# Kernel tuning notes

Measured on AMD Instinct MI355X. Metric: run time of the kernel, lower is better.

The kernel has to match this reference:

```python
import jax, jax.numpy as jnp
import numpy as np

B, S, H, NH, L, INTER, WIN = 2, 2048, 512, 8, 4, 2048, 64
HD = H // NH
W1 = WIN // 2          # one-sided window
WB = 2 * W1 + 1        # band width per query
EPS = 1e-12


def layer_norm(x, g, b):
    m = jnp.mean(x, axis=-1, keepdims=True)
    v = jnp.var(x, axis=-1, keepdims=True)
    return (x - m) / jnp.sqrt(v + EPS) * g + b


def setup_inputs() -> dict:
    key = jax.random.key(0)
    ks = jax.random.split(key, 12)
    std = 0.02
    n = lambda k, sh: jax.random.normal(k, sh, jnp.float32) * std
    return {
        "input_embs": jax.random.normal(ks[0], (B, S, H), jnp.float32),
        "attention_mask": jnp.ones((B, S), jnp.float32),
        "pos_emb": n(ks[1], (S, H)),
        "ln_emb_g": jnp.ones((H,), jnp.float32),
        "ln_emb_b": jnp.zeros((H,), jnp.float32),
        "Wq": n(ks[2], (L, H, H)), "bq": jnp.zeros((L, H), jnp.float32),
        "Wk": n(ks[3], (L, H, H)), "bk": jnp.zeros((L, H), jnp.float32),
        "Wv": n(ks[4], (L, H, H)), "bv": jnp.zeros((L, H), jnp.float32),
        "Wo": n(ks[5], (L, H, H)), "bo": jnp.zeros((L, H), jnp.float32),
        "ln1_g": jnp.ones((L, H), jnp.float32), "ln1_b": jnp.zeros((L, H), jnp.float32),
        "Wi": n(ks[6], (L, H, INTER)), "bi": jnp.zeros((L, INTER), jnp.float32),
        "Wo2": n(ks[7], (L, INTER, H)), "bo2": jnp.zeros((L, H), jnp.float32),
        "ln2_g": jnp.ones((L, H), jnp.float32), "ln2_b": jnp.zeros((L, H), jnp.float32),
        "pool_W1": n(ks[8], (H, H)), "pool_b1": jnp.zeros((H,), jnp.float32),
        "pool_W2": n(ks[9], (H, 1)), "pool_b2": jnp.zeros((1,), jnp.float32),
    }


def reference(input_embs, attention_mask, pos_emb, ln_emb_g, ln_emb_b,
              Wq, bq, Wk, bk, Wv, bv, Wo, bo, ln1_g, ln1_b,
              Wi, bi, Wo2, bo2, ln2_g, ln2_b,
              pool_W1, pool_b1, pool_W2, pool_b2):
    # extended additive mask: 0 for attend, -10000 for pad (no global tokens)
    ext = (1.0 - attention_mask) * -10000.0          # [B,S]
    is_masked = ext < 0                              # masked query positions

    # embeddings: input + position, LayerNorm (dropout is identity in eval)
    x = layer_norm(input_embs + pos_emb[None], ln_emb_g, ln_emb_b)

    # sliding-window band indices
    offs = jnp.arange(-W1, W1 + 1)
    idx = jnp.arange(S)[:, None] + offs[None, :]     # [S,WB]
    valid = (idx >= 0) & (idx < S)
    idxc = jnp.clip(idx, 0, S - 1)
    key_bias = ext[:, idxc]                          # [B,S,WB] additive key mask
    scale = 1.0 / jnp.sqrt(jnp.float32(HD))

    def layer(h, p):
        (wq, bq_, wk, bk_, wv, bv_, wo, bo_, g1, b1,
         wi, bi_, wo2, bo2_, g2, b2) = p
        q = (h @ wq + bq_).reshape(B, S, NH, HD) * scale
        k = (h @ wk + bk_).reshape(B, S, NH, HD)
        v = (h @ wv + bv_).reshape(B, S, NH, HD)
        kb = k[:, idxc]                              # [B,S,WB,NH,HD]
        vb = v[:, idxc]
        sc = jnp.einsum('bshd,bswhd->bhsw', q, kb) + key_bias[:, None]
        sc = jnp.where(valid[None, None], sc, -jnp.inf)
        pr = jax.nn.softmax(sc, axis=-1)
        pr = jnp.where(is_masked[:, None, :, None], 0.0, pr)
        ctx = jnp.einsum('bhsw,bswhd->bshd', pr, vb).reshape(B, S, H)
        attn = layer_norm(ctx @ wo + bo_ + h, g1, b1)          # BertSelfOutput
        inter = jax.nn.gelu(attn @ wi + bi_, approximate=False)  # BertIntermediate
        out = layer_norm(inter @ wo2 + bo2_ + attn, g2, b2)      # BertOutput
        return out, None

    params = (Wq, bq, Wk, bk, Wv, bv, Wo, bo, ln1_g, ln1_b,
              Wi, bi, Wo2, bo2, ln2_g, ln2_b)
    x, _ = jax.lax.scan(jax.checkpoint(layer), x, params)

    # AttentionPooling
    e = jnp.tanh(x @ pool_W1 + pool_b1)
    alpha = jnp.exp(e @ pool_W2 + pool_b2) * attention_mask[..., None]  # [B,S,1]
    alpha = alpha / (jnp.sum(alpha, axis=1, keepdims=True) + 1e-8)
    return jnp.einsum('bsh,bs->bh', x, alpha[..., 0])  # [B,H]
```

## Files before the change

kernel.cpp:

```cpp
#include <hip/hip_runtime.h>
#include <hip/hip_bf16.h>
#include <math.h>

#define B_ 2
#define S_ 2048
#define H_ 512
#define NH_ 8
#define HD_ 64
#define L_ 4
#define INTER_ 2048
#define W1_ 32
#define WB_ 65
#define M_ (B_*S_)

typedef __attribute__((ext_vector_type(8))) short short8v;
typedef __attribute__((ext_vector_type(4))) float f32x4;

__device__ __forceinline__ float b2f(ushort u){ return __uint_as_float(((unsigned)u)<<16); }
__device__ __forceinline__ ushort f2b(float f){
  unsigned u = __float_as_uint(f);
  unsigned r = (u + 0x7fffu + ((u>>16)&1u)) >> 16;
  return (ushort)r;
}

__device__ __forceinline__ void async16(const ushort* g, ushort* l){
  __builtin_amdgcn_global_load_lds(
      (const __attribute__((address_space(1))) unsigned int*)g,
      (__attribute__((address_space(3))) unsigned int*)l, 16, 0, 0);
}

__device__ __forceinline__ void tr_tile(const float* __restrict__ src,
    ushort* __restrict__ dst, int R, int C, int r0, int c0)
{
  __shared__ ushort tile[32][33];
  int tx = threadIdx.x & 31, ty = threadIdx.x >> 5;
  #pragma unroll
  for (int i = 0; i < 4; ++i){
    int r = r0 + ty + i*8;
    tile[ty + i*8][tx] = f2b(src[(size_t)r * C + c0 + tx]);
  }
  __syncthreads();
  #pragma unroll
  for (int i = 0; i < 4; ++i){
    int c = c0 + ty + i*8;
    dst[(size_t)c * R + r0 + tx] = tile[tx][ty + i*8];
  }
}

struct TPack {
  const float* wq; const float* wk; const float* wv;
  const float* wo; const float* pw1;
  ushort* wqkvT; ushort* woT; ushort* pw1T;
};

__global__ __launch_bounds__(256) void transpose512_all(TPack p)
{
  int z = blockIdx.z;
  const float* src; ushort* dst;
  if (z < 12){
    int kind = z >> 2, l = z & 3;
    const float* s3[3] = {p.wq, p.wk, p.wv};
    src = s3[kind] + (size_t)l*512*512;
    dst = p.wqkvT + (size_t)l*1536*512 + (size_t)kind*512*512;
  } else if (z < 16){
    int l = z - 12;
    src = p.wo + (size_t)l*512*512;
    dst = p.woT + (size_t)l*512*512;
  } else {
    src = p.pw1; dst = p.pw1T;
  }
  tr_tile(src, dst, 512, 512, blockIdx.y*32, blockIdx.x*32);
}

__global__ __launch_bounds__(256) void transpose_k(const float* __restrict__ src,
    ushort* __restrict__ dst, int R, int C, size_t sBatch, size_t dBatch)
{
  src += (size_t)blockIdx.z * sBatch;
  dst += (size_t)blockIdx.z * dBatch;
  tr_tile(src, dst, R, C, blockIdx.y*32, blockIdx.x*32);
}

__global__ __launch_bounds__(256) void pack_bqkv(const float* __restrict__ bq,
    const float* __restrict__ bk, const float* __restrict__ bv, float* __restrict__ dst)
{
  int i = blockIdx.x * 256 + threadIdx.x;
  int l = i / 1536, n = i % 1536;
  float v = (n < 512) ? bq[l*512 + n] : (n < 1024 ? bk[l*512 + n - 512] : bv[l*512 + n - 1024]);
  dst[i] = v;
}

template<int EPI, int BM>
__global__ __launch_bounds__(256, (BM == 64) ? 4 : 3) void gemm_bt(
    const ushort* __restrict__ A, const ushort* __restrict__ Bt,
    const float* __restrict__ bias, ushort* __restrict__ o16,
    float* __restrict__ o32, int M, int N, int K, int Klen)
{
  constexpr int ABUF = BM * 32;
  constexpr int BUFE = ABUF + 4096;
  constexpr int MI = BM / 32;
  constexpr int AL = BM / 64;
  __shared__ ushort lds[3 * BUFE];
  const int tid = threadIdx.x;
  const int bm = blockIdx.y * BM, bn = blockIdx.x * 128;
  const int kbeg = blockIdx.z * Klen;
  const int wave = tid >> 6, lane = tid & 63;
  const int wr = (wave >> 1) * (BM / 2), wc = (wave & 1) * 64;
  const int lr = lane & 15, lg = lane >> 4;
  const int lkS = (lg ^ ((lr >> 1) & 3)) * 8;
  f32x4 acc[MI][4] = {};

  const int srow = tid >> 2;
  const int schk = (((tid & 3) ^ ((tid >> 3) & 3))) * 8;
  const ushort* Ag  = A  + (size_t)(bm + srow) * K + kbeg + schk;
  const ushort* Bg0 = Bt + (size_t)(bn + srow) * K + kbeg + schk;
  const ushort* Bg1 = Bt + (size_t)(bn + 64 + srow) * K + kbeg + schk;

  const int nIter = Klen >> 5;
  auto issueTile = [&](int t, int buf){
    int k0 = t << 5;
    ushort* d = &lds[0] + buf*BUFE + tid*8;
    #pragma unroll
    for (int r = 0; r < AL; ++r)
      async16(Ag + (size_t)r*64*K + k0, d + r*2048);
    async16(Bg0 + k0, d + ABUF);
    async16(Bg1 + k0, d + ABUF + 2048);
  };

  issueTile(0, 0);
  issueTile(1, 1);

  int cb = 0;
  for (int t = 0; t < nIter; ++t){
    int ib = cb + 2; if (ib >= 3) ib -= 3;
    if (t + 2 < nIter) issueTile(t + 2, ib);
    if constexpr (BM == 64){
      if (t + 2 < nIter)      asm volatile("s_waitcnt vmcnt(6)" ::: "memory");
      else if (t + 1 < nIter) asm volatile("s_waitcnt vmcnt(3)" ::: "memory");
      else                    asm volatile("s_waitcnt vmcnt(0)" ::: "memory");
    } else {
      if (t + 2 < nIter)      asm volatile("s_waitcnt vmcnt(8)" ::: "memory");
      else if (t + 1 < nIter) asm volatile("s_waitcnt vmcnt(4)" ::: "memory");
      else                    asm volatile("s_waitcnt vmcnt(0)" ::: "memory");
    }
    __builtin_amdgcn_sched_barrier(0);
    __builtin_amdgcn_s_barrier();
    const ushort* bufp = &lds[0] + cb*BUFE;
    short8v af[MI], bfr[4];
    #pragma unroll
    for (int mi = 0; mi < MI; ++mi)
      af[mi] = *(const short8v*)(bufp + (wr + mi*16 + lr)*32 + lkS);
    #pragma unroll
    for (int nj = 0; nj < 4; ++nj)
      bfr[nj] = *(const short8v*)(bufp + ABUF + (wc + nj*16 + lr)*32 + lkS);
    #pragma unroll
    for (int mi = 0; mi < MI; ++mi)
      #pragma unroll
      for (int nj = 0; nj < 4; ++nj)
        acc[mi][nj] = __builtin_amdgcn_mfma_f32_16x16x32_bf16(af[mi], bfr[nj], acc[mi][nj], 0, 0, 0);
    __builtin_amdgcn_s_barrier();
    cb = cb + 1; if (cb == 3) cb = 0;
  }

  const float bscale = (blockIdx.z == 0) ? 1.0f : 0.0f;
  #pragma unroll
  for (int mi = 0; mi < MI; ++mi){
    #pragma unroll
    for (int nj = 0; nj < 4; ++nj){
      int col = bn + wc + nj*16 + lr;
      float bv = bias[col] * bscale;
      #pragma unroll
      for (int j = 0; j < 4; ++j){
        int row = bm + wr + mi*16 + lg*4 + j;
        float v = acc[mi][nj][j] + bv;
        if (EPI == 1) v = 0.5f * v * (1.0f + erff(v * 0.70710678118654752f));
        if (EPI == 2) v = tanhf(v);
        if (EPI == 3) o32[(size_t)blockIdx.z*M*N + (size_t)row * N + col] = v;
        else          o16[(size_t)row * N + col] = f2b(v);
      }
    }
  }
}

__device__ __forceinline__ void block_ln_stats(float v0, float v1, float* red,
                                               float& mean, float& rstd)
{
  int tid = threadIdx.x, wave = tid >> 6, lane = tid & 63;
  float sm = v0 + v1;
  float sq = v0*v0 + v1*v1;
  #pragma unroll
  for (int o = 32; o > 0; o >>= 1){ sm += __shfl_xor(sm, o); sq += __shfl_xor(sq, o); }
  if (lane == 0){ red[wave] = sm; red[4 + wave] = sq; }
  __syncthreads();
  float S = red[0] + red[1] + red[2] + red[3];
  float Q = red[4] + red[5] + red[6] + red[7];
  mean = S * (1.0f / 512.0f);
  float var = Q * (1.0f / 512.0f) - mean*mean;
  if (var < 0.f) var = 0.f;
  rstd = rsqrtf(var + 1e-12f);
}

__global__ __launch_bounds__(256) void embed_ln(const float* __restrict__ x,
    const float* __restrict__ pos, const float* __restrict__ g,
    const float* __restrict__ bb, ushort* __restrict__ out16, float* __restrict__ out32)
{
  __shared__ float red[8];
  int row = blockIdx.x, tid = threadIdx.x;
  int s = row & (S_ - 1);
  const size_t base = (size_t)row*H_ + tid*2;
  float2 xv = *(const float2*)(x + base);
  float2 pv = *(const float2*)(pos + (size_t)s*H_ + tid*2);
  float v0 = xv.x + pv.x, v1 = xv.y + pv.y;
  float mean, rstd;
  block_ln_stats(v0, v1, red, mean, rstd);
  float2 gv = *(const float2*)(g + tid*2);
  float2 bv = *(const float2*)(bb + tid*2);
  float r0 = (v0 - mean)*rstd*gv.x + bv.x;
  float r1 = (v1 - mean)*rstd*gv.y + bv.y;
  ushort2 o2; o2.x = f2b(r0); o2.y = f2b(r1);
  *(ushort2*)(out16 + base) = o2;
  float2 f2v; f2v.x = r0; f2v.y = r1;
  *(float2*)(out32 + base) = f2v;
}

__global__ __launch_bounds__(256) void ln_res(const float* __restrict__ t,
    const float* __restrict__ res, const float* __restrict__ g,
    const float* __restrict__ bb, ushort* __restrict__ out16, float* __restrict__ out32)
{
  __shared__ float red[8];
  int row = blockIdx.x, tid = threadIdx.x;
  const size_t MN = (size_t)M_*H_;
  const size_t base = (size_t)row*H_ + tid*2;
  float2 t0 = *(const float2*)(t + base);
  float2 t1v = *(const float2*)(t + MN + base);
  float2 rv = *(const float2*)(res + base);
  float v0 = t0.x + t1v.x + rv.x;
  float v1 = t0.y + t1v.y + rv.y;
  float mean, rstd;
  block_ln_stats(v0, v1, red, mean, rstd);
  float2 gv = *(const float2*)(g + tid*2);
  float2 bv = *(const float2*)(bb + tid*2);
  float r0 = (v0 - mean)*rstd*gv.x + bv.x;
  float r1 = (v1 - mean)*rstd*gv.y + bv.y;
  ushort2 o2; o2.x = f2b(r0); o2.y = f2b(r1);
  *(ushort2*)(out16 + base) = o2;
  float2 f2v; f2v.x = r0; f2v.y = r1;
  *(float2*)(out32 + base) = f2v;
}

__global__ __launch_bounds__(256) void attn_mfma(const ushort* __restrict__ qkv,
    const float* __restrict__ mask, ushort* __restrict__ ctx)
{
  __shared__ ushort K_lds[128][72];
  __shared__ ushort Vt[64][136];
  __shared__ ushort P_lds[64][136];
  __shared__ float  kb[128];

  const int tid = threadIdx.x, wave = tid >> 6, lane = tid & 63;
  const int hh = blockIdx.y & (NH_ - 1), b = blockIdx.y >> 3;
  const int s0 = blockIdx.x * 64;
  const size_t rb = (size_t)b * S_;

  const int ch = tid & 7;
  const int rr = tid >> 3;
  #pragma unroll
  for (int it = 0; it < 2; ++it){
    int c0 = rr*2 + it*64;
    short8v vv[2];
    #pragma unroll
    for (int p = 0; p < 2; ++p){
      int c = c0 + p;
      int j = s0 - 32 + c;
      int jc = min(max(j, 0), S_ - 1);
      const size_t rowb = (rb + jc) * 1536 + hh*64 + ch*8;
      *(short8v*)(&K_lds[c][ch*8]) = *(const short8v*)(qkv + rowb + 512);
      vv[p] = *(const short8v*)(qkv + rowb + 1024);
    }
    #pragma unroll
    for (int t = 0; t < 8; ++t){
      int tt = (t + ch) & 7;
      int d = ch*8 + tt;
      ushort2 w; w.x = (ushort)vv[0][tt]; w.y = (ushort)vv[1][tt];
      *(ushort2*)(&Vt[d][c0]) = w;
    }
  }
  if (tid < 128){
    int j = s0 - 32 + tid;
    kb[tid] = (j >= 0 && j < S_) ? (1.0f - mask[rb + j]) * (-10000.0f) : -1e30f;
  }
  __syncthreads();

  const int wq0 = wave * 16;
  const int lr = lane & 15, lg = lane >> 4, lk = lg * 8;

  const ushort* qbase = qkv + (rb + s0 + wq0 + lr) * 1536 + hh*64;
  short8v aq0 = *(const short8v*)(qbase + lk);
  short8v aq1 = *(const short8v*)(qbase + 32 + lk);

  f32x4 sacc[8];
  #pragma unroll
  for (int cn = 0; cn < 8; ++cn){
    short8v bk0 = *(const short8v*)(&K_lds[cn*16 + lr][lk]);
    short8v bk1 = *(const short8v*)(&K_lds[cn*16 + lr][32 + lk]);
    f32x4 z = {0.f, 0.f, 0.f, 0.f};
    z = __builtin_amdgcn_mfma_f32_16x16x32_bf16(aq0, bk0, z, 0, 0, 0);
    z = __builtin_amdgcn_mfma_f32_16x16x32_bf16(aq1, bk1, z, 0, 0, 0);
    sacc[cn] = z;
  }

  #pragma unroll
  for (int jr = 0; jr < 4; ++jr){
    const int R = wq0 + lg*4 + jr;
    float v[8], mx = -1e30f;
    #pragma unroll
    for (int cn = 0; cn < 8; ++cn){
      int c = cn*16 + lr;
      float sc = sacc[cn][jr] * 0.125f + kb[c];
      if (c < R || c > R + 64) sc = -1e30f;
      v[cn] = sc;
      mx = fmaxf(mx, sc);
    }
    #pragma unroll
    for (int o = 1; o < 16; o <<= 1) mx = fmaxf(mx, __shfl_xor(mx, o));
    float sum = 0.f;
    #pragma unroll
    for (int cn = 0; cn < 8; ++cn){ v[cn] = __expf(v[cn] - mx); sum += v[cn]; }
    #pragma unroll
    for (int o = 1; o < 16; o <<= 1) sum += __shfl_xor(sum, o);
    float qm = mask[rb + s0 + R];
    float inv = ((qm < 0.999f) ? 0.0f : 1.0f) / sum;
    #pragma unroll
    for (int cn = 0; cn < 8; ++cn)
      P_lds[R][cn*16 + lr] = f2b(v[cn] * inv);
  }

  short8v ap[4];
  #pragma unroll
  for (int ks = 0; ks < 4; ++ks)
    ap[ks] = *(const short8v*)(&P_lds[wq0 + lr][ks*32 + lk]);
  #pragma unroll
  for (int dn = 0; dn < 4; ++dn){
    f32x4 z = {0.f, 0.f, 0.f, 0.f};
    #pragma unroll
    for (int ks = 0; ks < 4; ++ks){
      short8v bv = *(const short8v*)(&Vt[dn*16 + lr][ks*32 + lk]);
      z = __builtin_amdgcn_mfma_f32_16x16x32_bf16(ap[ks], bv, z, 0, 0, 0);
    }
    #pragma unroll
    for (int jr = 0; jr < 4; ++jr){
      int R = wq0 + lg*4 + jr;
      ctx[(rb + s0 + R)*H_ + hh*64 + dn*16 + lr] = f2b(z[jr]);
    }
  }
}

__global__ __launch_bounds__(256) void pool_logit(const ushort* __restrict__ e,
    const float* __restrict__ w2, const float* __restrict__ b2p,
    const float* __restrict__ mask, float* __restrict__ alpha)
{
  int tid = threadIdx.x, wave = tid >> 6, lane = tid & 63;
  int r = blockIdx.x * 4 + wave;
  short8v ev = *(const short8v*)(e + (size_t)r*H_ + lane*8);
  float sacc = 0.f;
  #pragma unroll
  for (int j = 0; j < 8; ++j) sacc += b2f((ushort)ev[j]) * w2[lane*8 + j];
  #pragma unroll
  for (int o = 32; o > 0; o >>= 1) sacc += __shfl_xor(sacc, o);
  if (lane == 0){
    float logit = sacc + b2p[0];
    alpha[r] = __expf(logit) * mask[r];
  }
}

__global__ __launch_bounds__(256) void pool_sum(const float* __restrict__ alpha,
                                                float* __restrict__ invsum)
{
  __shared__ float red[4];
  int b = blockIdx.x, tid = threadIdx.x, wave = tid >> 6, lane = tid & 63;
  float s = 0.f;
  for (int k = tid; k < S_; k += 256) s += alpha[b*S_ + k];
  #pragma unroll
  for (int o = 32; o > 0; o >>= 1) s += __shfl_xor(s, o);
  if (lane == 0) red[wave] = s;
  __syncthreads();
  if (tid == 0) invsum[b] = 1.0f / (red[0] + red[1] + red[2] + red[3] + 1e-8f);
}

__global__ __launch_bounds__(256) void pool_wsum(const float* __restrict__ x,
    const float* __restrict__ alpha, float* __restrict__ out_acc)
{
  int chunk = blockIdx.x, b = blockIdx.y, tid = threadIdx.x;
  int s0 = chunk * 128;
  int c0 = tid * 2;
  float a0 = 0.f, a1 = 0.f;
  for (int i = 0; i < 128; ++i){
    int srow = s0 + i;
    float al = alpha[b*S_ + srow];
    float2 xv = *(const float2*)(x + (size_t)(b*S_ + srow)*H_ + c0);
    a0 += xv.x * al;
    a1 += xv.y * al;
  }
  float2 o; o.x = a0; o.y = a1;
  *(float2*)(out_acc + (size_t)chunk*B_*H_ + b*H_ + c0) = o;
}

__global__ __launch_bounds__(256) void pool_final(const float* __restrict__ out_acc,
    const float* __restrict__ invsum, float* __restrict__ out)
{
  int i = blockIdx.x * 256 + threadIdx.x;
  if (i < B_*H_){
    int b = i >> 9;
    float s = 0.f;
    #pragma unroll
    for (int c = 0; c < 16; ++c) s += out_acc[(size_t)c*B_*H_ + i];
    out[i] = s * invsum[b];
  }
}

extern "C" void kernel_launch(void* const* d_in, const int* in_sizes, int n_in,
                              void* d_out, int out_size, void* d_ws, size_t ws_size,
                              hipStream_t stream)
{
  const float* input_embs = (const float*)d_in[0];
  const float* mask       = (const float*)d_in[1];
  const float* pos        = (const float*)d_in[2];
  const float* ln_emb_g   = (const float*)d_in[3];
  const float* ln_emb_b   = (const float*)d_in[4];
  const float* Wq  = (const float*)d_in[5];
  const float* bq  = (const float*)d_in[6];
  const float* Wk  = (const float*)d_in[7];
  const float* bk  = (const float*)d_in[8];
  const float* Wv  = (const float*)d_in[9];
  const float* bv  = (const float*)d_in[10];
  const float* Wo  = (const float*)d_in[11];
  const float* bo  = (const float*)d_in[12];
  const float* ln1_g = (const float*)d_in[13];
  const float* ln1_b = (const float*)d_in[14];
  const float* Wi  = (const float*)d_in[15];
  const float* bi  = (const float*)d_in[16];
  const float* Wo2 = (const float*)d_in[17];
  const float* bo2 = (const float*)d_in[18];
  const float* ln2_g = (const float*)d_in[19];
  const float* ln2_b = (const float*)d_in[20];
  const float* pW1 = (const float*)d_in[21];
  const float* pb1 = (const float*)d_in[22];
  const float* pW2 = (const float*)d_in[23];
  const float* pb2 = (const float*)d_in[24];

  char* ws = (char*)d_ws;
  size_t off = 0;
  auto alloc = [&](size_t bytes)->char*{
    char* p = ws + off; off += (bytes + 255) & ~(size_t)255; return p;
  };
  ushort* WqkvT  = (ushort*)alloc((size_t)L_*1536*512*2);
  ushort* WoT    = (ushort*)alloc((size_t)L_*512*512*2);
  ushort* WiT    = (ushort*)alloc((size_t)L_*2048*512*2);
  ushort* Wo2T   = (ushort*)alloc((size_t)L_*512*2048*2);
  ushort* pW1T   = (ushort*)alloc((size_t)512*512*2);
  float*  bqkv   = (float*)alloc((size_t)L_*1536*4);
  ushort* h16    = (ushort*)alloc((size_t)M_*H_*2);
  float*  h32    = (float*)alloc((size_t)M_*H_*4);
  ushort* qkv    = (ushort*)alloc((size_t)M_*1536*2);
  ushort* ctx    = (ushort*)alloc((size_t)M_*H_*2);
  ushort* attn16 = (ushort*)alloc((size_t)M_*H_*2);
  float*  attn32 = (float*)alloc((size_t)M_*H_*4);
  ushort* inter  = (ushort*)alloc((size_t)M_*INTER_*2);
  float*  t1     = (float*)alloc((size_t)2*M_*H_*4);
  float*  alpha  = (float*)alloc((size_t)M_*4);
  float*  invsum = (float*)alloc(256);
  float*  outacc = (float*)alloc((size_t)16*B_*H_*4);

  dim3 tb(256);
  TPack tp;
  tp.wq = Wq; tp.wk = Wk; tp.wv = Wv; tp.wo = Wo; tp.pw1 = pW1;
  tp.wqkvT = WqkvT; tp.woT = WoT; tp.pw1T = pW1T;
  transpose512_all<<<dim3(16,16,17), tb, 0, stream>>>(tp);
  transpose_k<<<dim3(64,16,L_), tb, 0, stream>>>(Wi, WiT,    512, 2048, (size_t)512*2048, (size_t)2048*512);
  transpose_k<<<dim3(16,64,L_), tb, 0, stream>>>(Wo2, Wo2T, 2048,  512, (size_t)2048*512, (size_t)512*2048);
  pack_bqkv<<<dim3(L_*1536/256), tb, 0, stream>>>(bq, bk, bv, bqkv);

  embed_ln<<<dim3(M_), tb, 0, stream>>>(input_embs, pos, ln_emb_g, ln_emb_b, h16, h32);

  for (int l = 0; l < L_; ++l){
    gemm_bt<0,64><<<dim3(12,64,1), tb, 0, stream>>>(h16, WqkvT + (size_t)l*1536*512, bqkv + l*1536,
                                                    qkv, nullptr, M_, 1536, 512, 512);
    attn_mfma<<<dim3(S_/64, B_*NH_), tb, 0, stream>>>(qkv, mask, ctx);
    gemm_bt<3,64><<<dim3(4,64,2), tb, 0, stream>>>(ctx, WoT + (size_t)l*512*512, bo + l*512,
                                                   nullptr, t1, M_, 512, 512, 256);
    ln_res<<<dim3(M_), tb, 0, stream>>>(t1, h32, ln1_g + l*512, ln1_b + l*512, attn16, attn32);
    gemm_bt<1,128><<<dim3(16,32,1), tb, 0, stream>>>(attn16, WiT + (size_t)l*2048*512, bi + l*2048,
                                                     inter, nullptr, M_, 2048, 512, 512);
    gemm_bt<3,64><<<dim3(4,64,2), tb, 0, stream>>>(inter, Wo2T + (size_t)l*512*2048, bo2 + l*512,
                                                   nullptr, t1, M_, 512, 2048, 1024);
    ln_res<<<dim3(M_), tb, 0, stream>>>(t1, attn32, ln2_g + l*512, ln2_b + l*512, h16, h32);
  }

  gemm_bt<2,64><<<dim3(4,64,1), tb, 0, stream>>>(h16, pW1T, pb1, ctx, nullptr, M_, 512, 512, 512);
  pool_logit<<<dim3(M_/4), tb, 0, stream>>>(ctx, pW2, pb2, mask, alpha);
  pool_sum<<<dim3(B_), tb, 0, stream>>>(alpha, invsum);
  pool_wsum<<<dim3(16, B_), tb, 0, stream>>>(h32, alpha, outacc);
  pool_final<<<dim3((B_*H_ + 255)/256), tb, 0, stream>>>(outacc, invsum, (float*)d_out);
}
```

Baseline: 403.6 us.

## Switch GEMM to BK=64 double-buffered LDS pipeline with XOR swizzle

Reworks the bf16 MFMA GEMM main loop. It moves from a 3-stage ring buffer with K-tile 32 to a 2-stage double buffer with K-tile 64, using an 8-chunk XOR swizzle for the LDS layout. Each iteration now issues the next tile's async loads, runs two MFMA k-substeps on the current buffer, then waits for all loads and synchronises once. The aim is fewer barriers and waitcnts per unit of K work; the cost is more LDS per block, lower occupancy bounds (3/2 instead of 4/3) and a shallower prefetch distance.

```diff
diff --git a/kernel.cpp b/kernel.cpp
--- a/kernel.cpp
+++ b/kernel.cpp
@@ -90,75 +90,80 @@
 }
 
 template<int EPI, int BM>
-__global__ __launch_bounds__(256, (BM == 64) ? 4 : 3) void gemm_bt(
+__global__ __launch_bounds__(256, (BM == 64) ? 3 : 2) void gemm_bt(
     const ushort* __restrict__ A, const ushort* __restrict__ Bt,
     const float* __restrict__ bias, ushort* __restrict__ o16,
     float* __restrict__ o32, int M, int N, int K, int Klen)
 {
-  constexpr int ABUF = BM * 32;
-  constexpr int BUFE = ABUF + 4096;
+  constexpr int ABUF = BM * 64;
+  constexpr int BUFE = ABUF + 128 * 64;
   constexpr int MI = BM / 32;
-  constexpr int AL = BM / 64;
-  __shared__ ushort lds[3 * BUFE];
+  constexpr int AR = (BM * 8) / 256;
+  constexpr int BR = 4;
+  __shared__ ushort lds[2 * BUFE];
   const int tid = threadIdx.x;
   const int bm = blockIdx.y * BM, bn = blockIdx.x * 128;
   const int kbeg = blockIdx.z * Klen;
   const int wave = tid >> 6, lane = tid & 63;
   const int wr = (wave >> 1) * (BM / 2), wc = (wave & 1) * 64;
   const int lr = lane & 15, lg = lane >> 4;
-  const int lkS = (lg ^ ((lr >> 1) & 3)) * 8;
+  const int l7 = lr & 7;
   f32x4 acc[MI][4] = {};
 
-  const int srow = tid >> 2;
-  const int schk = (((tid & 3) ^ ((tid >> 3) & 3))) * 8;
-  const ushort* Ag  = A  + (size_t)(bm + srow) * K + kbeg + schk;
-  const ushort* Bg0 = Bt + (size_t)(bn + srow) * K + kbeg + schk;
-  const ushort* Bg1 = Bt + (size_t)(bn + 64 + srow) * K + kbeg + schk;
-
-  const int nIter = Klen >> 5;
+  const ushort* srcA[AR];
+  const ushort* srcB[BR];
+  #pragma unroll
+  for (int ra = 0; ra < AR; ++ra){
+    int s = tid + ra*256; int r = s >> 3, g = s & 7;
+    srcA[ra] = A + (size_t)(bm + r) * K + kbeg + (g ^ (r & 7)) * 8;
+  }
+  #pragma unroll
+  for (int rb = 0; rb < BR; ++rb){
+    int s = tid + rb*256; int r = s >> 3, g = s & 7;
+    srcB[rb] = Bt + (size_t)(bn + r) * K + kbeg + (g ^ (r & 7)) * 8;
+  }
+
+  const int nIter = Klen >> 6;
   auto issueTile = [&](int t, int buf){
-    int k0 = t << 5;
-    ushort* d = &lds[0] + buf*BUFE + tid*8;
-    #pragma unroll
-    for (int r = 0; r < AL; ++r)
-      async16(Ag + (size_t)r*64*K + k0, d + r*2048);
-    async16(Bg0 + k0, d + ABUF);
-    async16(Bg1 + k0, d + ABUF + 2048);
+    int k0 = t << 6;
+    ushort* dA = &lds[0] + buf*BUFE + tid*8;
+    ushort* dB = &lds[0] + buf*BUFE + ABUF + tid*8;
+    #pragma unroll
+    for (int ra = 0; ra < AR; ++ra) async16(srcA[ra] + k0, dA + ra*2048);
+    #pragma unroll
+    for (int rb = 0; rb < BR; ++rb) async16(srcB[rb] + k0, dB + rb*2048);
   };
 
   issueTile(0, 0);
-  issueTile(1, 1);
-
-  int cb = 0;
+  asm volatile("s_waitcnt vmcnt(0)" ::: "memory");
+  __builtin_amdgcn_s_barrier();
+
+  int cur = 0;
   for (int t = 0; t < nIter; ++t){
-    int ib = cb + 2; if (ib >= 3) ib -= 3;
-    if (t + 2 < nIter) issueTile(t + 2, ib);
-    if constexpr (BM == 64){
-      if (t + 2 < nIter)      asm volatile("s_waitcnt vmcnt(6)" ::: "memory");
-      else if (t + 1 < nIter) asm volatile("s_waitcnt vmcnt(3)" ::: "memory");
-      else                    asm volatile("s_waitcnt vmcnt(0)" ::: "memory");
-    } else {
-      if (t + 2 < nIter)      asm volatile("s_waitcnt vmcnt(8)" ::: "memory");
-      else if (t + 1 < nIter) asm volatile("s_waitcnt vmcnt(4)" ::: "memory");
-      else                    asm volatile("s_waitcnt vmcnt(0)" ::: "memory");
-    }
-    __builtin_amdgcn_sched_barrier(0);
+    if (t + 1 < nIter) issueTile(t + 1, cur ^ 1);
+    const ushort* bufp = &lds[0] + cur*BUFE;
+    #pragma unroll
+    for (int ks = 0; ks < 2; ++ks){
+      short8v af[MI], bfr[4];
+      #pragma unroll
+      for (int mi = 0; mi < MI; ++mi){
+        int R = wr + mi*16 + lr;
+        af[mi] = *(const short8v*)(bufp + R*64 + (((ks*4 + lg) ^ l7) * 8));
+      }
+      #pragma unroll
+      for (int nj = 0; nj < 4; ++nj){
+        int Rb = wc + nj*16 + lr;
+        bfr[nj] = *(const short8v*)(bufp + ABUF + Rb*64 + (((ks*4 + lg) ^ l7) * 8));
+      }
+      #pragma unroll
+      for (int mi = 0; mi < MI; ++mi)
+        #pragma unroll
+        for (int nj = 0; nj < 4; ++nj)
+          acc[mi][nj] = __builtin_amdgcn_mfma_f32_16x16x32_bf16(af[mi], bfr[nj], acc[mi][nj], 0, 0, 0);
+    }
+    asm volatile("s_waitcnt vmcnt(0)" ::: "memory");
     __builtin_amdgcn_s_barrier();
-    const ushort* bufp = &lds[0] + cb*BUFE;
-    short8v af[MI], bfr[4];
-    #pragma unroll
-    for (int mi = 0; mi < MI; ++mi)
-      af[mi] = *(const short8v*)(bufp + (wr + mi*16 + lr)*32 + lkS);
-    #pragma unroll
-    for (int nj = 0; nj < 4; ++nj)
-      bfr[nj] = *(const short8v*)(bufp + ABUF + (wc + nj*16 + lr)*32 + lkS);
-    #pragma unroll
-    for (int mi = 0; mi < MI; ++mi)
-      #pragma unroll
-      for (int nj = 0; nj < 4; ++nj)
-        acc[mi][nj] = __builtin_amdgcn_mfma_f32_16x16x32_bf16(af[mi], bfr[nj], acc[mi][nj], 0, 0, 0);
-    __builtin_amdgcn_s_barrier();
-    cb = cb + 1; if (cb == 3) cb = 0;
+    cur ^= 1;
   }
 
   const float bscale = (blockIdx.z == 0) ? 1.0f : 0.0f;
```

After: 402.3 us. No clear change (-0.3%).
